# Performance work log

Measured on AMD Instinct MI355X. Metric: run time of the kernel, lower is better.

Reference implementation:

```python
import jax, jax.numpy as jnp
import numpy as np

N = 100000      # nodes
E = 1600000     # edges (avg degree 16)
IN = 128        # in_size
H = 4           # num_heads
DH = 16         # hid_size (per-head)
DO = 16         # out_size (per-head)
NEG_SLOPE = 0.2 # DGL GATConv default leaky_relu slope


def setup_inputs():
    key = jax.random.key(0)
    ks = jax.random.split(key, 12)
    s = 0.1
    return {
        "x":   jax.random.normal(ks[0], (N, IN), jnp.float32),
        "src": jax.random.randint(ks[1], (E,), 0, N, jnp.int32),
        "dst": jax.random.randint(ks[2], (E,), 0, N, jnp.int32),
        # layer 1: in=128 -> H*DH=64, residual Linear (128 != 64)
        "W1":    jax.random.normal(ks[3], (IN, H * DH), jnp.float32) * s,
        "al1":   jax.random.normal(ks[4], (H, DH), jnp.float32) * s,
        "ar1":   jax.random.normal(ks[5], (H, DH), jnp.float32) * s,
        "resW1": jax.random.normal(ks[6], (IN, H * DH), jnp.float32) * s,
        "b1":    jnp.zeros((H * DH,), jnp.float32),
        # layer 2: in=H*DH=64 -> H*DO=64, residual is Identity reshape (64 == 64)
        "W2":  jax.random.normal(ks[7], (H * DH, H * DO), jnp.float32) * s,
        "al2": jax.random.normal(ks[8], (H, DO), jnp.float32) * s,
        "ar2": jax.random.normal(ks[9], (H, DO), jnp.float32) * s,
        "b2":  jnp.zeros((H * DO,), jnp.float32),
    }


def gat_layer(h, W, al, ar, res, bias, src, dst):
    """One DGL-style GATConv (no internal activation). Returns [N, H, D]."""
    d = W.shape[1] // H
    feat = (h @ W).reshape(-1, H, d)                       # [N,H,D]
    el = jnp.einsum('nhd,hd->nh', feat, al)                # [N,H]
    er = jnp.einsum('nhd,hd->nh', feat, ar)                # [N,H]
    e = jax.nn.leaky_relu(el[src] + er[dst], NEG_SLOPE)    # [E,H]
    # segment softmax over incoming edges of each destination node
    emax = jax.lax.stop_gradient(jax.ops.segment_max(e, dst, num_segments=N))
    ee = jnp.exp(e - emax[dst])                            # [E,H]
    den = jax.ops.segment_sum(ee, dst, num_segments=N)     # [N,H]
    alpha = ee / den[dst]                                  # [E,H]
    msg = alpha[:, :, None] * feat[src]                    # [E,H,D]
    out = jax.ops.segment_sum(msg, dst, num_segments=N)    # [N,H,D]
    return out + res + bias.reshape(1, H, d)


def reference(x, src, dst, W1, al1, ar1, resW1, b1, W2, al2, ar2, b2):
    # layer 1 (residual via Linear since IN != H*DH)
    res1 = (x @ resW1).reshape(N, H, DH)
    h = gat_layer(x, W1, al1, ar1, res1, b1, src, dst)     # [N,H,DH]
    h = jax.nn.elu(h.reshape(N, H * DH))                   # flatten + elu (dropout=eval identity)
    # layer 2 (identity residual since H*DH == H*DO)
    res2 = h.reshape(N, H, DO)
    h = gat_layer(h, W2, al2, ar2, res2, b2, src, dst)     # [N,H,DO]
    return h.mean(axis=1)                                  # [N,DO]
```

## Files before the change

kernel.cpp:

```cpp
#include <hip/hip_runtime.h>
#include <hip/hip_bf16.h>

static inline int cdiv(int a, int b){ return (a+b-1)/b; }

#define LEAKY(x) ((x) >= 0.f ? (x) : 0.2f*(x))

#define NBK   256
#define NBKSH 8
#define CAP   5120

__device__ inline unsigned short bf16bits(float f){
  __hip_bfloat16 h = __float2bfloat16(f);
  return *reinterpret_cast<unsigned short*>(&h);
}


__global__ __launch_bounds__(256) void binA(const int* __restrict__ src,
    const int* __restrict__ dst, int* __restrict__ acur, unsigned int* __restrict__ tmp,
    int E, int B, int epb)
{
  __shared__ int cnt1[512], cnt2[512], gbase[512];
  const int tid = threadIdx.x;
  for (int j = tid; j < 512; j += 256) { cnt1[j] = 0; cnt2[j] = 0; }
  __syncthreads();
  const int beg = blockIdx.x*epb, end = min(E, beg+epb);
  for (int e = beg+tid; e < end; e += 256) atomicAdd(&cnt1[dst[e]>>NBKSH], 1);
  __syncthreads();
  for (int j = tid; j < B; j += 256) gbase[j] = atomicAdd(&acur[j], cnt1[j]);
  __syncthreads();
  for (int e = beg+tid; e < end; e += 256) {
    int s = src[e], d = dst[e];
    int b = d >> NBKSH;
    int tk = atomicAdd(&cnt2[b], 1);
    int slot = gbase[b] + tk;
    if (slot < CAP)
      tmp[(size_t)b*CAP + slot] = ((unsigned)s << NBKSH) | (unsigned)(d & (NBK-1));
  }
}


__global__ __launch_bounds__(512) void bucket_scan(const int* __restrict__ acur,
    int* __restrict__ bbase, int* __restrict__ off, int B, int N, int E)
{
  __shared__ int wsum[8];
  const int tid = threadIdx.x, lane = tid & 63, wave = tid >> 6;
  int v = (tid < B) ? acur[tid] : 0;
  int x = v;
  #pragma unroll
  for (int s = 1; s < 64; s <<= 1) { int t = __shfl_up(x, s); if (lane >= s) x += t; }
  if (lane == 63) wsum[wave] = x;
  __syncthreads();
  if (tid == 0) { int r = 0; for (int w = 0; w < 8; w++) { int t = wsum[w]; wsum[w] = r; r += t; } }
  __syncthreads();
  int excl = wsum[wave] + x - v;
  if (tid < B)    bbase[tid] = excl;
  if (tid == B-1) bbase[B]   = excl + v;
  if (tid == 0)   off[N]     = E;
}


__global__ __launch_bounds__(256) void binC(const unsigned int* __restrict__ tmp,
    const int* __restrict__ acur, const int* __restrict__ bbase,
    int* __restrict__ off, int2* __restrict__ csr, int N)
{
  __shared__ int sA[NBK], sB[NBK];
  const int b = blockIdx.x, tid = threadIdx.x;
  const int m = min(acur[b], CAP);
  const int base = bbase[b];
  const int n0 = b*NBK;
  const int nn = min(NBK, N - n0);
  if (tid < NBK) sA[tid] = 0;
  __syncthreads();
  const unsigned int* tb = tmp + (size_t)b*CAP;
  for (int i = tid; i < m; i += 256) atomicAdd(&sA[tb[i] & (NBK-1)], 1);
  __syncthreads();
  int* in = sA; int* ob = sB;
  for (int st = 1; st < NBK; st <<= 1) {
    if (tid < NBK) { int v = in[tid]; if (tid >= st) v += in[tid-st]; ob[tid] = v; }
    __syncthreads();
    int* t = in; in = ob; ob = t;
  }
  if (tid < NBK) ob[tid] = tid ? in[tid-1] : 0;
  __syncthreads();
  if (tid < nn) off[n0 + tid] = base + ob[tid];
  __syncthreads();
  for (int i = tid; i < m; i += 256) {
    unsigned v = tb[i];
    int local = v & (NBK-1);
    int pos = atomicAdd(&ob[local], 1);
    csr[base + pos] = int2{(int)(v >> NBKSH), n0 + local};
  }
}


template<bool ATTN, bool BF16OUT>
__global__ __launch_bounds__(256) void lin128(const float* __restrict__ X,
    const float* __restrict__ W, const float* __restrict__ al, const float* __restrict__ ar,
    void* __restrict__ featout, float* __restrict__ el, float* __restrict__ er, int n)
{
  __shared__ float Ws[128*64];
  __shared__ float Xs[32*129];
  const int tid = threadIdx.x;
  const int nbase = blockIdx.x * 32;
  for (int i = tid; i < 128*64/4; i += 256) ((float4*)Ws)[i] = ((const float4*)W)[i];
  for (int idx = tid; idx < 32*32; idx += 256) {
    int node = idx >> 5, fq = idx & 31;
    int gn = nbase + node;
    float4 v = (gn < n) ? ((const float4*)X)[(size_t)gn*32 + fq] : float4{0.f,0.f,0.f,0.f};
    Xs[node*129 + fq*4 + 0] = v.x;
    Xs[node*129 + fq*4 + 1] = v.y;
    Xs[node*129 + fq*4 + 2] = v.z;
    Xs[node*129 + fq*4 + 3] = v.w;
  }
  __syncthreads();
  const int c0 = (tid & 15) * 4;
  const int n0 = (tid >> 4) * 2;
  float a00=0,a01=0,a02=0,a03=0, a10=0,a11=0,a12=0,a13=0;
  #pragma unroll 4
  for (int k = 0; k < 128; k++) {
    float4 w = *(const float4*)&Ws[k*64 + c0];
    float x0 = Xs[n0*129 + k];
    float x1 = Xs[n0*129 + 129 + k];
    a00 = fmaf(x0, w.x, a00); a01 = fmaf(x0, w.y, a01);
    a02 = fmaf(x0, w.z, a02); a03 = fmaf(x0, w.w, a03);
    a10 = fmaf(x1, w.x, a10); a11 = fmaf(x1, w.y, a11);
    a12 = fmaf(x1, w.z, a12); a13 = fmaf(x1, w.w, a13);
  }
  const int g0 = nbase + n0, g1 = g0 + 1;
  if (BF16OUT) {
    unsigned short* fb = (unsigned short*)featout;
    if (g0 < n) *(ushort4*)&fb[(size_t)g0*64 + c0] = ushort4{bf16bits(a00),bf16bits(a01),bf16bits(a02),bf16bits(a03)};
    if (g1 < n) *(ushort4*)&fb[(size_t)g1*64 + c0] = ushort4{bf16bits(a10),bf16bits(a11),bf16bits(a12),bf16bits(a13)};
  } else {
    float* fb = (float*)featout;
    if (g0 < n) *(float4*)&fb[(size_t)g0*64 + c0] = float4{a00,a01,a02,a03};
    if (g1 < n) *(float4*)&fb[(size_t)g1*64 + c0] = float4{a10,a11,a12,a13};
  }
  if (ATTN) {
    float l0=al[c0], l1=al[c0+1], l2=al[c0+2], l3=al[c0+3];
    float r0=ar[c0], r1=ar[c0+1], r2=ar[c0+2], r3=ar[c0+3];
    float e0 = a00*l0 + a01*l1 + a02*l2 + a03*l3;
    float e1 = a10*l0 + a11*l1 + a12*l2 + a13*l3;
    float q0 = a00*r0 + a01*r1 + a02*r2 + a03*r3;
    float q1 = a10*r0 + a11*r1 + a12*r2 + a13*r3;
    e0 += __shfl_xor(e0,1); e0 += __shfl_xor(e0,2);
    e1 += __shfl_xor(e1,1); e1 += __shfl_xor(e1,2);
    q0 += __shfl_xor(q0,1); q0 += __shfl_xor(q0,2);
    q1 += __shfl_xor(q1,1); q1 += __shfl_xor(q1,2);
    if ((tid & 3) == 0) {
      int h = (tid & 15) >> 2;
      if (g0 < n) { el[g0*4+h] = e0; er[g0*4+h] = q0; }
      if (g1 < n) { el[g1*4+h] = e1; er[g1*4+h] = q1; }
    }
  }
}


__global__ __launch_bounds__(256) void lin64(const float* __restrict__ X,
    const float* __restrict__ W, const float* __restrict__ al, const float* __restrict__ ar,
    unsigned short* __restrict__ feat, float* __restrict__ el, float* __restrict__ er, int n)
{
  __shared__ float Ws[64*64];
  __shared__ float Xs[64*65];
  const int tid = threadIdx.x;
  const int nbase = blockIdx.x * 64;
  for (int i = tid; i < 64*64/4; i += 256) ((float4*)Ws)[i] = ((const float4*)W)[i];
  for (int idx = tid; idx < 64*16; idx += 256) {
    int node = idx >> 4, fq = idx & 15;
    int gn = nbase + node;
    float4 v = (gn < n) ? ((const float4*)X)[(size_t)gn*16 + fq] : float4{0.f,0.f,0.f,0.f};
    Xs[node*65 + fq*4 + 0] = v.x;
    Xs[node*65 + fq*4 + 1] = v.y;
    Xs[node*65 + fq*4 + 2] = v.z;
    Xs[node*65 + fq*4 + 3] = v.w;
  }
  __syncthreads();
  const int c0 = (tid & 15) * 4;
  const int n0 = (tid >> 4) * 4;
  float acc[4][4];
  #pragma unroll
  for (int i = 0; i < 4; i++)
    #pragma unroll
    for (int j = 0; j < 4; j++) acc[i][j] = 0.f;
  #pragma unroll 4
  for (int k = 0; k < 64; k++) {
    float4 w = *(const float4*)&Ws[k*64 + c0];
    #pragma unroll
    for (int i = 0; i < 4; i++) {
      float x = Xs[(n0+i)*65 + k];
      acc[i][0] = fmaf(x, w.x, acc[i][0]);
      acc[i][1] = fmaf(x, w.y, acc[i][1]);
      acc[i][2] = fmaf(x, w.z, acc[i][2]);
      acc[i][3] = fmaf(x, w.w, acc[i][3]);
    }
  }
  float l0=al[c0], l1=al[c0+1], l2=al[c0+2], l3=al[c0+3];
  float r0=ar[c0], r1=ar[c0+1], r2=ar[c0+2], r3=ar[c0+3];
  #pragma unroll
  for (int i = 0; i < 4; i++) {
    int g = nbase + n0 + i;
    if (g < n) *(ushort4*)&feat[(size_t)g*64 + c0] =
        ushort4{bf16bits(acc[i][0]),bf16bits(acc[i][1]),bf16bits(acc[i][2]),bf16bits(acc[i][3])};
    float e = acc[i][0]*l0 + acc[i][1]*l1 + acc[i][2]*l2 + acc[i][3]*l3;
    float q = acc[i][0]*r0 + acc[i][1]*r1 + acc[i][2]*r2 + acc[i][3]*r3;
    e += __shfl_xor(e,1); e += __shfl_xor(e,2);
    q += __shfl_xor(q,1); q += __shfl_xor(q,2);
    if ((tid & 3) == 0 && g < n) {
      int h = (tid & 15) >> 2;
      el[g*4+h] = e; er[g*4+h] = q;
    }
  }
}


__global__ __launch_bounds__(256) void score_kernel(const int2* __restrict__ csr,
    const float* __restrict__ el, const float* __restrict__ er,
    float* __restrict__ alpha, int E4)
{
  int t = blockIdx.x*256 + threadIdx.x;
  if (t >= E4) return;
  int i = t >> 2, h = t & 3;
  int2 sd = csr[i];
  float e = el[sd.x*4 + h] + er[sd.y*4 + h];
  alpha[t] = __expf(LEAKY(e));
}


template<int LAYER>
__global__ __launch_bounds__(256) void aggregate_fused(const int* __restrict__ off,
    const int2* __restrict__ csr, const float* __restrict__ alpha,
    const __hip_bfloat16* __restrict__ feat, const float* __restrict__ res,
    const float* __restrict__ bias, float* __restrict__ out, int n)
{
  const int wave = threadIdx.x >> 6, lane = threadIdx.x & 63;
  const int node = blockIdx.x*4 + wave;
  if (node >= n) return;
  const int h = lane >> 4;
  const int beg = off[node], end = off[node+1];
  float d[8], a[8];
  #pragma unroll
  for (int k = 0; k < 8; k++) { d[k] = 0.f; a[k] = 0.f; }
  int i = beg;
  for (; i + 8 <= end; i += 8) {
    int   s[8]; float p[8], f[8];
    #pragma unroll
    for (int k = 0; k < 8; k++) s[k] = csr[i+k].x;
    #pragma unroll
    for (int k = 0; k < 8; k++) p[k] = alpha[(i+k)*4 + h];
    #pragma unroll
    for (int k = 0; k < 8; k++) f[k] = __bfloat162float(feat[(size_t)s[k]*64 + lane]);
    #pragma unroll
    for (int k = 0; k < 8; k++) { d[k] += p[k]; a[k] = fmaf(p[k], f[k], a[k]); }
  }
  for (; i < end; i++) {
    int s = csr[i].x;
    float p = alpha[i*4 + h];
    d[0] += p;
    a[0] = fmaf(p, __bfloat162float(feat[(size_t)s*64 + lane]), a[0]);
  }
  float den = ((d[0]+d[1])+(d[2]+d[3])) + ((d[4]+d[5])+(d[6]+d[7]));
  float acc = ((a[0]+a[1])+(a[2]+a[3])) + ((a[4]+a[5])+(a[6]+a[7]));
  float v = (den > 0.f) ? (acc/den) : 0.f;
  v += res[(size_t)node*64 + lane] + bias[lane];
  if (LAYER == 1) {
    v = (v > 0.f) ? v : expm1f(v);
    out[(size_t)node*64 + lane] = v;
  } else {
    v += __shfl_xor(v, 16);
    v += __shfl_xor(v, 32);
    if (lane < 16) out[(size_t)node*16 + lane] = 0.25f*v;
  }
}


extern "C" void kernel_launch(void* const* d_in, const int* in_sizes, int n_in,
                              void* d_out, int out_size, void* d_ws, size_t ws_size,
                              hipStream_t stream)
{
  (void)n_in; (void)out_size; (void)ws_size;
  const float* x   = (const float*)d_in[0];
  const int*   src = (const int*)  d_in[1];
  const int*   dst = (const int*)  d_in[2];
  const float* W1  = (const float*)d_in[3];
  const float* al1 = (const float*)d_in[4];
  const float* ar1 = (const float*)d_in[5];
  const float* rW1 = (const float*)d_in[6];
  const float* b1  = (const float*)d_in[7];
  const float* W2  = (const float*)d_in[8];
  const float* al2 = (const float*)d_in[9];
  const float* ar2 = (const float*)d_in[10];
  const float* b2  = (const float*)d_in[11];
  float* out = (float*)d_out;

  const int N_ = in_sizes[0] / 128;
  const int E_ = in_sizes[1];
  const int B_ = cdiv(N_, NBK);

  char* ws = (char*)d_ws;
  size_t o = 0;
  auto alloc = [&](size_t bytes)->char* {
    char* p = ws + o; o += (bytes + 255) & ~(size_t)255; return p;
  };
  int*   acur    = (int*)  alloc((size_t)B_*4);
  int*   bbase   = (int*)  alloc(((size_t)B_+1)*4);
  int*   off     = (int*)  alloc(((size_t)N_+1)*4);
  unsigned int* tmp = (unsigned int*)alloc((size_t)B_*CAP*4);
  int2*  csr     = (int2*) alloc((size_t)E_*8);
  float* alpha   = (float*)alloc((size_t)E_*4*4);
  unsigned short* featb = (unsigned short*)alloc((size_t)N_*64*2);
  float* el      = (float*)alloc((size_t)N_*4*4);
  float* er      = (float*)alloc((size_t)N_*4*4);
  float* hbuf    = (float*)alloc((size_t)N_*64*4);

  hipMemsetAsync(acur, 0, (size_t)B_*4, stream);
  binA<<<256, 256, 0, stream>>>(src, dst, acur, tmp, E_, B_, cdiv(E_,256));
  bucket_scan<<<1, 512, 0, stream>>>(acur, bbase, off, B_, N_, E_);
  binC<<<B_, 256, 0, stream>>>(tmp, acur, bbase, off, csr, N_);

  lin128<true,  true ><<<cdiv(N_,32), 256, 0, stream>>>(x, W1,  al1, ar1, featb, el, er, N_);
  lin128<false, false><<<cdiv(N_,32), 256, 0, stream>>>(x, rW1, nullptr, nullptr, hbuf, nullptr, nullptr, N_);
  score_kernel<<<cdiv(E_*4,256), 256, 0, stream>>>(csr, el, er, alpha, E_*4);
  aggregate_fused<1><<<cdiv(N_,4), 256, 0, stream>>>(off, csr, alpha,
      (const __hip_bfloat16*)featb, hbuf, b1, hbuf, N_);

  lin64<<<cdiv(N_,64), 256, 0, stream>>>(hbuf, W2, al2, ar2, featb, el, er, N_);
  score_kernel<<<cdiv(E_*4,256), 256, 0, stream>>>(csr, el, er, alpha, E_*4);
  aggregate_fused<2><<<cdiv(N_,4), 256, 0, stream>>>(off, csr, alpha,
      (const __hip_bfloat16*)featb, hbuf, b2, out, N_);
}
```

Baseline: 436.5 us.

## Use head-major feature and score layouts, aggregate per head, and fuse the layer-1 GEMMs

```diff
diff --git a/kernel.cpp b/kernel.cpp
--- a/kernel.cpp
+++ b/kernel.cpp
@@ -93,16 +93,21 @@
 }
 
 
-template<bool ATTN, bool BF16OUT>
-__global__ __launch_bounds__(256) void lin128(const float* __restrict__ X,
-    const float* __restrict__ W, const float* __restrict__ al, const float* __restrict__ ar,
-    void* __restrict__ featout, float* __restrict__ el, float* __restrict__ er, int n)
+__global__ __launch_bounds__(256) void lin128_fused(const float* __restrict__ X,
+    const float* __restrict__ W, const float* __restrict__ RW,
+    const float* __restrict__ al, const float* __restrict__ ar,
+    unsigned short* __restrict__ featH, float* __restrict__ el, float* __restrict__ er,
+    float* __restrict__ res, int n, int N)
 {
   __shared__ float Ws[128*64];
+  __shared__ float Rs[128*64];
   __shared__ float Xs[32*129];
   const int tid = threadIdx.x;
   const int nbase = blockIdx.x * 32;
-  for (int i = tid; i < 128*64/4; i += 256) ((float4*)Ws)[i] = ((const float4*)W)[i];
+  for (int i = tid; i < 128*64/4; i += 256) {
+    ((float4*)Ws)[i] = ((const float4*)W)[i];
+    ((float4*)Rs)[i] = ((const float4*)RW)[i];
+  }
   for (int idx = tid; idx < 32*32; idx += 256) {
     int node = idx >> 5, fq = idx & 31;
     int gn = nbase + node;
@@ -115,50 +120,50 @@
   __syncthreads();
   const int c0 = (tid & 15) * 4;
   const int n0 = (tid >> 4) * 2;
-  float a00=0,a01=0,a02=0,a03=0, a10=0,a11=0,a12=0,a13=0;
+  float a0[4]={0,0,0,0}, a1[4]={0,0,0,0}, r0v[4]={0,0,0,0}, r1v[4]={0,0,0,0};
   #pragma unroll 4
   for (int k = 0; k < 128; k++) {
-    float4 w = *(const float4*)&Ws[k*64 + c0];
+    float4 w  = *(const float4*)&Ws[k*64 + c0];
+    float4 rw = *(const float4*)&Rs[k*64 + c0];
     float x0 = Xs[n0*129 + k];
     float x1 = Xs[n0*129 + 129 + k];
-    a00 = fmaf(x0, w.x, a00); a01 = fmaf(x0, w.y, a01);
-    a02 = fmaf(x0, w.z, a02); a03 = fmaf(x0, w.w, a03);
-    a10 = fmaf(x1, w.x, a10); a11 = fmaf(x1, w.y, a11);
-    a12 = fmaf(x1, w.z, a12); a13 = fmaf(x1, w.w, a13);
+    a0[0]=fmaf(x0,w.x,a0[0]);  a0[1]=fmaf(x0,w.y,a0[1]);  a0[2]=fmaf(x0,w.z,a0[2]);  a0[3]=fmaf(x0,w.w,a0[3]);
+    a1[0]=fmaf(x1,w.x,a1[0]);  a1[1]=fmaf(x1,w.y,a1[1]);  a1[2]=fmaf(x1,w.z,a1[2]);  a1[3]=fmaf(x1,w.w,a1[3]);
+    r0v[0]=fmaf(x0,rw.x,r0v[0]); r0v[1]=fmaf(x0,rw.y,r0v[1]); r0v[2]=fmaf(x0,rw.z,r0v[2]); r0v[3]=fmaf(x0,rw.w,r0v[3]);
+    r1v[0]=fmaf(x1,rw.x,r1v[0]); r1v[1]=fmaf(x1,rw.y,r1v[1]); r1v[2]=fmaf(x1,rw.z,r1v[2]); r1v[3]=fmaf(x1,rw.w,r1v[3]);
   }
   const int g0 = nbase + n0, g1 = g0 + 1;
-  if (BF16OUT) {
-    unsigned short* fb = (unsigned short*)featout;
-    if (g0 < n) *(ushort4*)&fb[(size_t)g0*64 + c0] = ushort4{bf16bits(a00),bf16bits(a01),bf16bits(a02),bf16bits(a03)};
-    if (g1 < n) *(ushort4*)&fb[(size_t)g1*64 + c0] = ushort4{bf16bits(a10),bf16bits(a11),bf16bits(a12),bf16bits(a13)};
-  } else {
-    float* fb = (float*)featout;
-    if (g0 < n) *(float4*)&fb[(size_t)g0*64 + c0] = float4{a00,a01,a02,a03};
-    if (g1 < n) *(float4*)&fb[(size_t)g1*64 + c0] = float4{a10,a11,a12,a13};
-  }
-  if (ATTN) {
-    float l0=al[c0], l1=al[c0+1], l2=al[c0+2], l3=al[c0+3];
-    float r0=ar[c0], r1=ar[c0+1], r2=ar[c0+2], r3=ar[c0+3];
-    float e0 = a00*l0 + a01*l1 + a02*l2 + a03*l3;
-    float e1 = a10*l0 + a11*l1 + a12*l2 + a13*l3;
-    float q0 = a00*r0 + a01*r1 + a02*r2 + a03*r3;
-    float q1 = a10*r0 + a11*r1 + a12*r2 + a13*r3;
-    e0 += __shfl_xor(e0,1); e0 += __shfl_xor(e0,2);
-    e1 += __shfl_xor(e1,1); e1 += __shfl_xor(e1,2);
-    q0 += __shfl_xor(q0,1); q0 += __shfl_xor(q0,2);
-    q1 += __shfl_xor(q1,1); q1 += __shfl_xor(q1,2);
-    if ((tid & 3) == 0) {
-      int h = (tid & 15) >> 2;
-      if (g0 < n) { el[g0*4+h] = e0; er[g0*4+h] = q0; }
-      if (g1 < n) { el[g1*4+h] = e1; er[g1*4+h] = q1; }
-    }
+  const int hh = c0 >> 4, cb = c0 & 15;
+  if (g0 < n) {
+    *(ushort4*)&featH[((size_t)hh*N + g0)*16 + cb] = ushort4{bf16bits(a0[0]),bf16bits(a0[1]),bf16bits(a0[2]),bf16bits(a0[3])};
+    *(float4*)&res[(size_t)g0*64 + c0] = float4{r0v[0],r0v[1],r0v[2],r0v[3]};
+  }
+  if (g1 < n) {
+    *(ushort4*)&featH[((size_t)hh*N + g1)*16 + cb] = ushort4{bf16bits(a1[0]),bf16bits(a1[1]),bf16bits(a1[2]),bf16bits(a1[3])};
+    *(float4*)&res[(size_t)g1*64 + c0] = float4{r1v[0],r1v[1],r1v[2],r1v[3]};
+  }
+  float l0=al[c0], l1=al[c0+1], l2=al[c0+2], l3=al[c0+3];
+  float q0=ar[c0], q1=ar[c0+1], q2=ar[c0+2], q3=ar[c0+3];
+  float e0 = a0[0]*l0 + a0[1]*l1 + a0[2]*l2 + a0[3]*l3;
+  float e1 = a1[0]*l0 + a1[1]*l1 + a1[2]*l2 + a1[3]*l3;
+  float u0 = a0[0]*q0 + a0[1]*q1 + a0[2]*q2 + a0[3]*q3;
+  float u1 = a1[0]*q0 + a1[1]*q1 + a1[2]*q2 + a1[3]*q3;
+  e0 += __shfl_xor(e0,1); e0 += __shfl_xor(e0,2);
+  e1 += __shfl_xor(e1,1); e1 += __shfl_xor(e1,2);
+  u0 += __shfl_xor(u0,1); u0 += __shfl_xor(u0,2);
+  u1 += __shfl_xor(u1,1); u1 += __shfl_xor(u1,2);
+  if ((tid & 3) == 0) {
+    int h = (tid & 15) >> 2;
+    if (g0 < n) { el[g0*4+h] = e0; er[g0*4+h] = u0; }
+    if (g1 < n) { el[g1*4+h] = e1; er[g1*4+h] = u1; }
   }
 }
 
 
 __global__ __launch_bounds__(256) void lin64(const float* __restrict__ X,
     const float* __restrict__ W, const float* __restrict__ al, const float* __restrict__ ar,
-    unsigned short* __restrict__ feat, float* __restrict__ el, float* __restrict__ er, int n)
+    unsigned short* __restrict__ featH, float* __restrict__ el, float* __restrict__ er,
+    int n, int N)
 {
   __shared__ float Ws[64*64];
   __shared__ float Xs[64*65];
@@ -196,10 +201,11 @@
   }
   float l0=al[c0], l1=al[c0+1], l2=al[c0+2], l3=al[c0+3];
   float r0=ar[c0], r1=ar[c0+1], r2=ar[c0+2], r3=ar[c0+3];
+  const int hh = c0 >> 4, cb = c0 & 15;
   #pragma unroll
   for (int i = 0; i < 4; i++) {
     int g = nbase + n0 + i;
-    if (g < n) *(ushort4*)&feat[(size_t)g*64 + c0] =
+    if (g < n) *(ushort4*)&featH[((size_t)hh*N + g)*16 + cb] =
         ushort4{bf16bits(acc[i][0]),bf16bits(acc[i][1]),bf16bits(acc[i][2]),bf16bits(acc[i][3])};
     float e = acc[i][0]*l0 + acc[i][1]*l1 + acc[i][2]*l2 + acc[i][3]*l3;
     float q = acc[i][0]*r0 + acc[i][1]*r1 + acc[i][2]*r2 + acc[i][3]*r3;
@@ -215,61 +221,81 @@
 
 __global__ __launch_bounds__(256) void score_kernel(const int2* __restrict__ csr,
     const float* __restrict__ el, const float* __restrict__ er,
-    float* __restrict__ alpha, int E4)
-{
-  int t = blockIdx.x*256 + threadIdx.x;
-  if (t >= E4) return;
-  int i = t >> 2, h = t & 3;
-  int2 sd = csr[i];
-  float e = el[sd.x*4 + h] + er[sd.y*4 + h];
-  alpha[t] = __expf(LEAKY(e));
+    float* __restrict__ alphaH, int E)
+{
+  int e = blockIdx.x*256 + threadIdx.x;
+  if (e >= E) return;
+  int2 sd = csr[e];
+  float4 l = *(const float4*)&el[sd.x*4];
+  float4 r = *(const float4*)&er[sd.y*4];
+  alphaH[(size_t)0*E + e] = __expf(LEAKY(l.x + r.x));
+  alphaH[(size_t)1*E + e] = __expf(LEAKY(l.y + r.y));
+  alphaH[(size_t)2*E + e] = __expf(LEAKY(l.z + r.z));
+  alphaH[(size_t)3*E + e] = __expf(LEAKY(l.w + r.w));
 }
 
 
 template<int LAYER>
-__global__ __launch_bounds__(256) void aggregate_fused(const int* __restrict__ off,
-    const int2* __restrict__ csr, const float* __restrict__ alpha,
-    const __hip_bfloat16* __restrict__ feat, const float* __restrict__ res,
-    const float* __restrict__ bias, float* __restrict__ out, int n)
+__global__ __launch_bounds__(256) void aggregateH(const int* __restrict__ off,
+    const int2* __restrict__ csr, const float* __restrict__ alphaH,
+    const __hip_bfloat16* __restrict__ featH, const float* __restrict__ res,
+    const float* __restrict__ bias, float* __restrict__ outp, int n, int N, int E)
 {
   const int wave = threadIdx.x >> 6, lane = threadIdx.x & 63;
-  const int node = blockIdx.x*4 + wave;
+  const int slot = blockIdx.x & 7;
+  const int h    = slot & 3;
+  const int j    = blockIdx.x >> 3;
+  const int node = (j*2 + (slot>>2))*4 + wave;
   if (node >= n) return;
-  const int h = lane >> 4;
+  const int eg = lane >> 4, d = lane & 15;
   const int beg = off[node], end = off[node+1];
-  float d[8], a[8];
-  #pragma unroll
-  for (int k = 0; k < 8; k++) { d[k] = 0.f; a[k] = 0.f; }
+  const __hip_bfloat16* ft = featH + (size_t)h*N*16;
+  const float* ap = alphaH + (size_t)h*E;
+  float acc0=0.f, den0=0.f, acc1=0.f, den1=0.f;
   int i = beg;
   for (; i + 8 <= end; i += 8) {
-    int   s[8]; float p[8], f[8];
-    #pragma unroll
-    for (int k = 0; k < 8; k++) s[k] = csr[i+k].x;
-    #pragma unroll
-    for (int k = 0; k < 8; k++) p[k] = alpha[(i+k)*4 + h];
-    #pragma unroll
-    for (int k = 0; k < 8; k++) f[k] = __bfloat162float(feat[(size_t)s[k]*64 + lane]);
-    #pragma unroll
-    for (int k = 0; k < 8; k++) { d[k] += p[k]; a[k] = fmaf(p[k], f[k], a[k]); }
-  }
-  for (; i < end; i++) {
-    int s = csr[i].x;
-    float p = alpha[i*4 + h];
-    d[0] += p;
-    a[0] = fmaf(p, __bfloat162float(feat[(size_t)s*64 + lane]), a[0]);
-  }
-  float den = ((d[0]+d[1])+(d[2]+d[3])) + ((d[4]+d[5])+(d[6]+d[7]));
-  float acc = ((a[0]+a[1])+(a[2]+a[3])) + ((a[4]+a[5])+(a[6]+a[7]));
+    int   s0 = csr[i+eg].x,   s1 = csr[i+4+eg].x;
+    float p0 = ap[i+eg],      p1 = ap[i+4+eg];
+    float f0 = __bfloat162float(ft[(size_t)s0*16 + d]);
+    float f1 = __bfloat162float(ft[(size_t)s1*16 + d]);
+    den0 += p0; acc0 = fmaf(p0, f0, acc0);
+    den1 += p1; acc1 = fmaf(p1, f1, acc1);
+  }
+  for (; i < end; i += 4) {
+    bool act = (i + eg) < end;
+    int   s = act ? csr[i+eg].x : 0;
+    float p = act ? ap[i+eg] : 0.f;
+    float f = __bfloat162float(ft[(size_t)s*16 + d]);
+    den0 += p; acc0 = fmaf(p, f, acc0);
+  }
+  float acc = acc0 + acc1, den = den0 + den1;
+  acc += __shfl_xor(acc,16); acc += __shfl_xor(acc,32);
+  den += __shfl_xor(den,16); den += __shfl_xor(den,32);
   float v = (den > 0.f) ? (acc/den) : 0.f;
-  v += res[(size_t)node*64 + lane] + bias[lane];
+  const int c = h*16 + d;
+  v += res[(size_t)node*64 + c] + bias[c];
   if (LAYER == 1) {
     v = (v > 0.f) ? v : expm1f(v);
-    out[(size_t)node*64 + lane] = v;
+    if (eg == 0) outp[(size_t)node*64 + c] = v;
   } else {
-    v += __shfl_xor(v, 16);
-    v += __shfl_xor(v, 32);
-    if (lane < 16) out[(size_t)node*16 + lane] = 0.25f*v;
-  }
+    if (eg == 0) outp[((size_t)h*N + node)*16 + d] = v;
+  }
+}
+
+
+__global__ __launch_bounds__(256) void combine_kernel(const float* __restrict__ outH,
+    float* __restrict__ out, int n, int N)
+{
+  int t = blockIdx.x*256 + threadIdx.x;
+  if (t >= n*4) return;
+  int node = t >> 2, q = t & 3;
+  float4 s{0.f,0.f,0.f,0.f};
+  #pragma unroll
+  for (int h = 0; h < 4; h++) {
+    float4 v = ((const float4*)(outH + ((size_t)h*N + node)*16))[q];
+    s.x += v.x; s.y += v.y; s.z += v.z; s.w += v.w;
+  }
+  ((float4*)(out + (size_t)node*16))[q] = float4{0.25f*s.x, 0.25f*s.y, 0.25f*s.z, 0.25f*s.w};
 }
 
 
@@ -306,25 +332,28 @@
   int*   off     = (int*)  alloc(((size_t)N_+1)*4);
   unsigned int* tmp = (unsigned int*)alloc((size_t)B_*CAP*4);
   int2*  csr     = (int2*) alloc((size_t)E_*8);
-  float* alpha   = (float*)alloc((size_t)E_*4*4);
-  unsigned short* featb = (unsigned short*)alloc((size_t)N_*64*2);
+  float* alphaH  = (float*)alloc((size_t)E_*4*4);
+  unsigned short* featH = (unsigned short*)alloc((size_t)N_*64*2);
   float* el      = (float*)alloc((size_t)N_*4*4);
   float* er      = (float*)alloc((size_t)N_*4*4);
   float* hbuf    = (float*)alloc((size_t)N_*64*4);
+  float* outH    = (float*)alloc((size_t)N_*64*4);
 
   hipMemsetAsync(acur, 0, (size_t)B_*4, stream);
-  binA<<<256, 256, 0, stream>>>(src, dst, acur, tmp, E_, B_, cdiv(E_,256));
+  binA<<<128, 256, 0, stream>>>(src, dst, acur, tmp, E_, B_, cdiv(E_,128));
   bucket_scan<<<1, 512, 0, stream>>>(acur, bbase, off, B_, N_, E_);
   binC<<<B_, 256, 0, stream>>>(tmp, acur, bbase, off, csr, N_);
 
-  lin128<true,  true ><<<cdiv(N_,32), 256, 0, stream>>>(x, W1,  al1, ar1, featb, el, er, N_);
-  lin128<false, false><<<cdiv(N_,32), 256, 0, stream>>>(x, rW1, nullptr, nullptr, hbuf, nullptr, nullptr, N_);
-  score_kernel<<<cdiv(E_*4,256), 256, 0, stream>>>(csr, el, er, alpha, E_*4);
-  aggregate_fused<1><<<cdiv(N_,4), 256, 0, stream>>>(off, csr, alpha,
-      (const __hip_bfloat16*)featb, hbuf, b1, hbuf, N_);
-
-  lin64<<<cdiv(N_,64), 256, 0, stream>>>(hbuf, W2, al2, ar2, featb, el, er, N_);
-  score_kernel<<<cdiv(E_*4,256), 256, 0, stream>>>(csr, el, er, alpha, E_*4);
-  aggregate_fused<2><<<cdiv(N_,4), 256, 0, stream>>>(off, csr, alpha,
-      (const __hip_bfloat16*)featb, hbuf, b2, out, N_);
-}
+  const int aggGrid = 8 * cdiv(N_, 8);
+
+  lin128_fused<<<cdiv(N_,32), 256, 0, stream>>>(x, W1, rW1, al1, ar1, featH, el, er, hbuf, N_, N_);
+  score_kernel<<<cdiv(E_,256), 256, 0, stream>>>(csr, el, er, alphaH, E_);
+  aggregateH<1><<<aggGrid, 256, 0, stream>>>(off, csr, alphaH,
+      (const __hip_bfloat16*)featH, hbuf, b1, hbuf, N_, N_, E_);
+
+  lin64<<<cdiv(N_,64), 256, 0, stream>>>(hbuf, W2, al2, ar2, featH, el, er, N_, N_);
+  score_kernel<<<cdiv(E_,256), 256, 0, stream>>>(csr, el, er, alphaH, E_);
+  aggregateH<2><<<aggGrid, 256, 0, stream>>>(off, csr, alphaH,
+      (const __hip_bfloat16*)featH, hbuf, b2, outH, N_, N_, E_);
+  combine_kernel<<<cdiv(N_*4,256), 256, 0, stream>>>(outH, out, N_, N_);
+}
```

After: 646.1 us. 48.0% more time.
